# Kernel tuning notes

Measured on AMD Instinct MI355X. Metric: run time of the kernel, lower is better.

Reference implementation:

```python
import jax, jax.numpy as jnp
import numpy as np

N_HEAD = 16
HEAD_DIM = 128  # n_embd // n_head
EPS = 1e-6
ROPE_BASE = 10000.0


def rmsnorm(x, w):
    rms = jnp.mean(x * x, axis=-1, keepdims=True)
    return w * (x * jax.lax.rsqrt(rms + EPS))


def rope_cache(T, head_dim):
    half = head_dim // 2
    inv_freq = 1.0 / (ROPE_BASE ** (jnp.arange(half, dtype=jnp.float32) / half))
    pos = jnp.arange(T, dtype=jnp.float32)
    freqs = pos[:, None] * inv_freq[None, :]  # [T, half]
    return jnp.cos(freqs), jnp.sin(freqs)


def apply_rope(x, cos, sin):
    # x: [B, H, T, D]; cos/sin: [T, D/2]
    half = x.shape[-1] // 2
    x1, x2 = x[..., :half], x[..., half:]
    return jnp.concatenate([x1 * cos - x2 * sin, x1 * sin + x2 * cos], axis=-1)


def setup_inputs() -> dict:
    key = jax.random.key(0)
    ks = jax.random.split(key, 8)
    B, T, C, Hid = 2, 2048, 2048, 5632
    s = 0.02
    return {
        "x": jax.random.normal(ks[0], (B, T, C), dtype=jnp.float32),
        "w_norm1": jnp.ones((C,), dtype=jnp.float32),
        "w_qkv": jax.random.normal(ks[1], (C, 3 * C), dtype=jnp.float32) * s,
        "w_proj": jax.random.normal(ks[2], (C, C), dtype=jnp.float32) * s,
        "w_norm2": jnp.ones((C,), dtype=jnp.float32),
        "w1": jax.random.normal(ks[3], (C, Hid), dtype=jnp.float32) * s,
        "w2": jax.random.normal(ks[4], (C, Hid), dtype=jnp.float32) * s,
        "w3": jax.random.normal(ks[5], (Hid, C), dtype=jnp.float32) * s,
    }


def reference(x, w_norm1, w_qkv, w_proj, w_norm2, w1, w2, w3):
    B, T, C = x.shape
    H, D = N_HEAD, HEAD_DIM

    # ---- attention branch ----
    h = rmsnorm(x, w_norm1)
    qkv = h @ w_qkv  # [B, T, 3C]
    q, k, v = jnp.split(qkv, 3, axis=-1)
    q = q.reshape(B, T, H, D).transpose(0, 2, 1, 3)  # [B,H,T,D]
    k = k.reshape(B, T, H, D).transpose(0, 2, 1, 3)
    v = v.reshape(B, T, H, D).transpose(0, 2, 1, 3)

    cos, sin = rope_cache(T, D)
    q = apply_rope(q, cos, sin)
    k = apply_rope(k, cos, sin)

    att = jnp.einsum('bhqd,bhkd->bhqk', q, k) / np.sqrt(D).astype(np.float32)
    causal = jnp.tril(jnp.ones((T, T), dtype=bool))
    att = jnp.where(causal, att, -jnp.inf)
    att = jax.nn.softmax(att, axis=-1)
    out = jnp.einsum('bhqk,bhkd->bhqd', att, v)
    out = out.transpose(0, 2, 1, 3).reshape(B, T, C)
    x = x + out @ w_proj

    # ---- SwiGLU MLP branch ----
    h2 = rmsnorm(x, w_norm2)
    x = x + (jax.nn.silu(h2 @ w1) * (h2 @ w2)) @ w3
    return x
```

## Files before the change

kernel.cpp:

```cpp
#include <hip/hip_runtime.h>

typedef short s16x8 __attribute__((ext_vector_type(8)));
typedef unsigned short u16;
typedef u16 u16x8 __attribute__((ext_vector_type(8)));
typedef u16 u16x4 __attribute__((ext_vector_type(4)));
typedef float f32x4 __attribute__((ext_vector_type(4)));

#define DEVINL __device__ __forceinline__

DEVINL u16 f2bf(float f) {
    unsigned u = __float_as_uint(f);
    u += 0x7FFFu + ((u >> 16) & 1u);
    return (u16)(u >> 16);
}
DEVINL float bf2f(u16 h) { return __uint_as_float((unsigned)h << 16); }

DEVINL void gl2lds16(const void* g, void* l) {
    __builtin_amdgcn_global_load_lds((const __attribute__((address_space(1))) void*)g,
                                     (__attribute__((address_space(3))) void*)l, 16, 0, 0);
}

__global__ __launch_bounds__(256) void tcast(
    const float* __restrict__ src, u16* __restrict__ dst, const int K, const int N)
{
    __shared__ float tile[32][33];
    const long k0 = (long)blockIdx.x * 32;
    const long n0 = (long)blockIdx.y * 32;
    const int tid = threadIdx.x;
    const int r = tid >> 3, c4 = (tid & 7) * 4;
    float4 v = *(const float4*)&src[(k0 + r) * N + n0 + c4];
    tile[r][c4] = v.x; tile[r][c4 + 1] = v.y; tile[r][c4 + 2] = v.z; tile[r][c4 + 3] = v.w;
    __syncthreads();
    u16x4 ov;
    ov[0] = f2bf(tile[c4][r]);     ov[1] = f2bf(tile[c4 + 1][r]);
    ov[2] = f2bf(tile[c4 + 2][r]); ov[3] = f2bf(tile[c4 + 3][r]);
    *(u16x4*)&dst[(n0 + r) * K + k0 + c4] = ov;
}

__global__ __launch_bounds__(256) void rmsnorm_cast(
    const float* __restrict__ x, const float* __restrict__ wn, u16* __restrict__ out)
{
    const int C = 2048;
    const long row = blockIdx.x;
    const int tid = threadIdx.x;
    const float4* xr = (const float4*)(x + row * C);
    float4 a = xr[tid * 2], b = xr[tid * 2 + 1];
    float ss = a.x*a.x + a.y*a.y + a.z*a.z + a.w*a.w
             + b.x*b.x + b.y*b.y + b.z*b.z + b.w*b.w;
#pragma unroll
    for (int m = 1; m < 64; m <<= 1) ss += __shfl_xor(ss, m);
    __shared__ float red[4];
    if ((tid & 63) == 0) red[tid >> 6] = ss;
    __syncthreads();
    float scale = rsqrtf((red[0] + red[1] + red[2] + red[3]) * (1.f / 2048.f) + 1e-6f);
    const float4* wr = (const float4*)wn;
    float4 wa = wr[tid * 2], wb = wr[tid * 2 + 1];
    u16x8 o;
    o[0] = f2bf(a.x * scale * wa.x); o[1] = f2bf(a.y * scale * wa.y);
    o[2] = f2bf(a.z * scale * wa.z); o[3] = f2bf(a.w * scale * wa.w);
    o[4] = f2bf(b.x * scale * wb.x); o[5] = f2bf(b.y * scale * wb.y);
    o[6] = f2bf(b.z * scale * wb.z); o[7] = f2bf(b.w * scale * wb.w);
    *(u16x8*)&out[row * C + tid * 8] = o;
}

template <int MODE>
__global__ __launch_bounds__(256, 2) void gemm128(
    const u16* __restrict__ A, const u16* __restrict__ Bt,
    const int N, const int K,
    float* __restrict__ outF, u16* __restrict__ outB,
    const float* __restrict__ resid)
{
    __shared__ u16 As[128 * 64];
    __shared__ u16 Bs[128 * 64];
    const int tid = threadIdx.x;
    const int lane = tid & 63;
    const int w = tid >> 6;
    const int wm = w >> 1, wn = w & 1;
    const int quad = lane >> 4, l16 = lane & 15;
    const long m0 = (long)blockIdx.x * 128;
    const long n0 = (long)blockIdx.y * 128;

    const u16* ga[4]; const u16* gb[4]; char* la[4]; char* lb[4];
#pragma unroll
    for (int rr = 0; rr < 4; ++rr) {
        int idx = rr * 256 + tid;
        int r = idx >> 3, j = idx & 7;
        int c = (j ^ (r & 7)) * 8;
        ga[rr] = A + (m0 + r) * K + c;
        gb[rr] = Bt + (n0 + r) * K + c;
        la[rr] = (char*)As + idx * 16;
        lb[rr] = (char*)Bs + idx * 16;
    }

    f32x4 acc[4][4] = {};

    for (int k0 = 0; k0 < K; k0 += 64) {
#pragma unroll
        for (int rr = 0; rr < 4; ++rr) {
            gl2lds16(ga[rr] + k0, la[rr]);
            gl2lds16(gb[rr] + k0, lb[rr]);
        }
        __syncthreads();
#pragma unroll
        for (int ks = 0; ks < 2; ++ks) {
            s16x8 af[4], bfv[4];
#pragma unroll
            for (int mt = 0; mt < 4; ++mt)
                af[mt] = *(const s16x8*)&As[(wm * 64 + mt * 16 + l16) * 64 +
                                            ((ks * 4 + quad) ^ (l16 & 7)) * 8];
#pragma unroll
            for (int nt = 0; nt < 4; ++nt)
                bfv[nt] = *(const s16x8*)&Bs[(wn * 64 + nt * 16 + l16) * 64 +
                                             ((ks * 4 + quad) ^ (l16 & 7)) * 8];
#pragma unroll
            for (int mt = 0; mt < 4; ++mt)
#pragma unroll
                for (int nt = 0; nt < 4; ++nt)
                    acc[mt][nt] = __builtin_amdgcn_mfma_f32_16x16x32_bf16(af[mt], bfv[nt], acc[mt][nt], 0, 0, 0);
        }
        __syncthreads();
    }

#pragma unroll
    for (int mt = 0; mt < 4; ++mt)
#pragma unroll
        for (int reg = 0; reg < 4; ++reg) {
            long row = m0 + wm * 64 + mt * 16 + quad * 4 + reg;
#pragma unroll
            for (int nt = 0; nt < 4; ++nt) {
                long col = n0 + wn * 64 + nt * 16 + l16;
                float v = acc[mt][nt][reg];
                if (MODE == 0) {
                    outB[row * N + col] = f2bf(v);
                } else {
                    outF[row * N + col] = resid[row * N + col] + v;
                }
            }
        }
}

__global__ __launch_bounds__(256, 2) void gemm_ffn(
    const u16* __restrict__ A, const u16* __restrict__ B1t, const u16* __restrict__ B2t,
    const int N, const int K, u16* __restrict__ outB)
{
    __shared__ u16 As[128 * 64];
    __shared__ u16 B1s[128 * 64];
    __shared__ u16 B2s[128 * 64];
    const int tid = threadIdx.x;
    const int lane = tid & 63;
    const int w = tid >> 6;
    const int wm = w >> 1, wn = w & 1;
    const int quad = lane >> 4, l16 = lane & 15;
    const long m0 = (long)blockIdx.x * 128;
    const long n0 = (long)blockIdx.y * 128;

    const u16* ga[4]; const u16* gb1[4]; const u16* gb2[4];
    char* la[4]; char* lb1[4]; char* lb2[4];
#pragma unroll
    for (int rr = 0; rr < 4; ++rr) {
        int idx = rr * 256 + tid;
        int r = idx >> 3, j = idx & 7;
        int c = (j ^ (r & 7)) * 8;
        ga[rr]  = A + (m0 + r) * K + c;
        gb1[rr] = B1t + (n0 + r) * K + c;
        gb2[rr] = B2t + (n0 + r) * K + c;
        la[rr]  = (char*)As + idx * 16;
        lb1[rr] = (char*)B1s + idx * 16;
        lb2[rr] = (char*)B2s + idx * 16;
    }

    f32x4 acc1[4][4] = {};
    f32x4 acc2[4][4] = {};

    for (int k0 = 0; k0 < K; k0 += 64) {
#pragma unroll
        for (int rr = 0; rr < 4; ++rr) {
            gl2lds16(ga[rr] + k0, la[rr]);
            gl2lds16(gb1[rr] + k0, lb1[rr]);
            gl2lds16(gb2[rr] + k0, lb2[rr]);
        }
        __syncthreads();
#pragma unroll
        for (int ks = 0; ks < 2; ++ks) {
            s16x8 af[4], b1f[4], b2f[4];
#pragma unroll
            for (int mt = 0; mt < 4; ++mt)
                af[mt] = *(const s16x8*)&As[(wm * 64 + mt * 16 + l16) * 64 +
                                            ((ks * 4 + quad) ^ (l16 & 7)) * 8];
#pragma unroll
            for (int nt = 0; nt < 4; ++nt) {
                b1f[nt] = *(const s16x8*)&B1s[(wn * 64 + nt * 16 + l16) * 64 +
                                              ((ks * 4 + quad) ^ (l16 & 7)) * 8];
                b2f[nt] = *(const s16x8*)&B2s[(wn * 64 + nt * 16 + l16) * 64 +
                                              ((ks * 4 + quad) ^ (l16 & 7)) * 8];
            }
#pragma unroll
            for (int mt = 0; mt < 4; ++mt)
#pragma unroll
                for (int nt = 0; nt < 4; ++nt) {
                    acc1[mt][nt] = __builtin_amdgcn_mfma_f32_16x16x32_bf16(af[mt], b1f[nt], acc1[mt][nt], 0, 0, 0);
                    acc2[mt][nt] = __builtin_amdgcn_mfma_f32_16x16x32_bf16(af[mt], b2f[nt], acc2[mt][nt], 0, 0, 0);
                }
        }
        __syncthreads();
    }

#pragma unroll
    for (int mt = 0; mt < 4; ++mt)
#pragma unroll
        for (int reg = 0; reg < 4; ++reg) {
            long row = m0 + wm * 64 + mt * 16 + quad * 4 + reg;
#pragma unroll
            for (int nt = 0; nt < 4; ++nt) {
                long col = n0 + wn * 64 + nt * 16 + l16;
                float g = acc1[mt][nt][reg];
                float s = g / (1.f + __expf(-g));
                outB[row * N + col] = f2bf(s * acc2[mt][nt][reg]);
            }
        }
}

__global__ __launch_bounds__(256) void rope_qk(
    const u16* __restrict__ qkv, u16* __restrict__ qT, u16* __restrict__ kT)
{
    const int row = blockIdx.x;
    const int t = row & 2047, b = row >> 11;
    const int tid = threadIdx.x;
    __shared__ u16 buf[4096];
    const u16* src = qkv + (long)row * 6144;
    u16x8 aa = *(const u16x8*)&src[tid * 8];
    u16x8 kk = *(const u16x8*)&src[2048 + tid * 8];
    *(u16x8*)&buf[tid * 8] = aa;
    *(u16x8*)&buf[2048 + tid * 8] = kk;
    __syncthreads();
    const int c = tid * 8;
    const int h = c >> 7, dh = c & 127;
    const bool first = dh < 64;
    const int pc = first ? (c + 64) : (c - 64);
    float cs[8], sn[8];
#pragma unroll
    for (int j = 0; j < 8; ++j) {
        float inv = __expf(-(float)((dh & 63) + j) * 0.14391156831212787f);
        float ang = (float)t * inv;
        cs[j] = cosf(ang); sn[j] = sinf(ang);
    }
    const long obase = ((long)(b * 16 + h) * 2048 + t) * 128 + dh;
#pragma unroll
    for (int part = 0; part < 2; ++part) {
        const int base = part * 2048;
        u16x8 mine = *(const u16x8*)&buf[base + c];
        u16x8 oth  = *(const u16x8*)&buf[base + pc];
        const float qs = part ? 1.f : 0.08838834764831845f;
        u16x8 o;
#pragma unroll
        for (int j = 0; j < 8; ++j) {
            float xv = bf2f(mine[j]), yv = bf2f(oth[j]);
            float ov = first ? (xv * cs[j] - yv * sn[j]) : (yv * sn[j] + xv * cs[j]);
            o[j] = f2bf(ov * qs);
        }
        u16* dst = part ? kT : qT;
        *(u16x8*)&dst[obase] = o;
    }
}

__global__ __launch_bounds__(256) void vtrans(
    const u16* __restrict__ qkv, u16* __restrict__ vT)
{
    const int bh = blockIdx.x;
    const int b = bh >> 4, h = bh & 15;
    const int t0 = blockIdx.y * 64, d0 = blockIdx.z * 64;
    __shared__ u16 tile[64 * 65];
    const int tid = threadIdx.x;
#pragma unroll
    for (int rr = 0; rr < 2; ++rr) {
        int idx = rr * 256 + tid;
        int r = idx >> 3, c = (idx & 7) * 8;
        u16x8 v = *(const u16x8*)&qkv[(long)(b * 2048 + t0 + r) * 6144 + 4096 + h * 128 + d0 + c];
#pragma unroll
        for (int j = 0; j < 8; ++j) tile[r * 65 + c + j] = v[j];
    }
    __syncthreads();
#pragma unroll
    for (int rr = 0; rr < 2; ++rr) {
        int idx = rr * 256 + tid;
        int dd = idx >> 3, cc = (idx & 7) * 8;
        u16x8 o;
#pragma unroll
        for (int j = 0; j < 8; ++j) o[j] = tile[(cc + j) * 65 + dd];
        *(u16x8*)&vT[((long)bh * 128 + d0 + dd) * 2048 + t0 + cc] = o;
    }
}

__global__ __launch_bounds__(256, 2) void attn_kernel(
    const u16* __restrict__ qT, const u16* __restrict__ kT,
    const u16* __restrict__ vT, u16* __restrict__ outT)
{
    const int T = 2048, D = 128;
    const int qt = gridDim.x - 1 - blockIdx.x;
    const int bh = blockIdx.y;
    const int tid = threadIdx.x, lane = tid & 63, w = tid >> 6;
    const int quad = lane >> 4, l16 = lane & 15;
    const int qrow = qt * 64 + w * 16;

    __shared__ u16 Ks[2][64 * 128];
    __shared__ u16 Vs[2][128 * 64];
    __shared__ u16 Ps[4][16 * 64];

    s16x8 aq[4];
    const u16* qb = qT + ((long)bh * T + qrow + l16) * D;
#pragma unroll
    for (int kk = 0; kk < 4; ++kk)
        aq[kk] = *(const s16x8*)&qb[kk * 32 + quad * 8];

    f32x4 o[8] = {};
    float mi[4] = {-INFINITY, -INFINITY, -INFINITY, -INFINITY};
    float li[4] = {0.f, 0.f, 0.f, 0.f};

    const u16* kg0 = kT + (long)bh * T * D;
    const u16* vg0 = vT + (long)bh * D * T;

    auto stage = [&](int kt, int b) {
        const int k0 = kt * 64;
#pragma unroll
        for (int rr = 0; rr < 4; ++rr) {
            int idx = rr * 256 + tid;
            int kr = idx >> 4, kj = idx & 15;
            gl2lds16(kg0 + (long)(k0 + kr) * D + ((kj ^ (kr & 15)) * 8),
                     (char*)Ks[b] + idx * 16);
            int vr = idx >> 3, vj = idx & 7;
            gl2lds16(vg0 + (long)vr * T + k0 + ((vj ^ (vr & 7)) * 8),
                     (char*)Vs[b] + idx * 16);
        }
    };

    stage(0, 0);

    for (int kt = 0; kt <= qt; ++kt) {
        __syncthreads();
        if (kt < qt) stage(kt + 1, (kt + 1) & 1);
        const u16* ks_ = Ks[kt & 1];
        const u16* vs_ = Vs[kt & 1];
        const int k0 = kt * 64;

        f32x4 sf[4] = {};
#pragma unroll
        for (int kk = 0; kk < 4; ++kk) {
#pragma unroll
            for (int nt = 0; nt < 4; ++nt) {
                s16x8 kb = *(const s16x8*)&ks_[(nt * 16 + l16) * 128 +
                                               ((kk * 4 + quad) ^ (l16 & 15)) * 8];
                sf[nt] = __builtin_amdgcn_mfma_f32_16x16x32_bf16(aq[kk], kb, sf[nt], 0, 0, 0);
            }
        }

        float S[4][4];
        if (kt == qt) {
#pragma unroll
            for (int nt = 0; nt < 4; ++nt) {
                int col = k0 + nt * 16 + l16;
#pragma unroll
                for (int reg = 0; reg < 4; ++reg) {
                    int row = qrow + quad * 4 + reg;
                    S[nt][reg] = (col <= row) ? sf[nt][reg] : -INFINITY;
                }
            }
        } else {
#pragma unroll
            for (int nt = 0; nt < 4; ++nt)
#pragma unroll
                for (int reg = 0; reg < 4; ++reg)
                    S[nt][reg] = sf[nt][reg];
        }

        float rm[4];
#pragma unroll
        for (int reg = 0; reg < 4; ++reg)
            rm[reg] = fmaxf(fmaxf(S[0][reg], S[1][reg]), fmaxf(S[2][reg], S[3][reg]));
#pragma unroll
        for (int m = 1; m < 16; m <<= 1)
#pragma unroll
            for (int reg = 0; reg < 4; ++reg)
                rm[reg] = fmaxf(rm[reg], __shfl_xor(rm[reg], m));

        float alpha[4], rs[4];
#pragma unroll
        for (int reg = 0; reg < 4; ++reg) {
            float mn = fmaxf(mi[reg], rm[reg]);
            alpha[reg] = __expf(mi[reg] - mn);
            mi[reg] = mn;
            rs[reg] = 0.f;
        }
#pragma unroll
        for (int nt = 0; nt < 4; ++nt)
#pragma unroll
            for (int reg = 0; reg < 4; ++reg) {
                float p = __expf(S[nt][reg] - mi[reg]);
                S[nt][reg] = p;
                rs[reg] += p;
            }
#pragma unroll
        for (int m = 1; m < 16; m <<= 1)
#pragma unroll
            for (int reg = 0; reg < 4; ++reg)
                rs[reg] += __shfl_xor(rs[reg], m);
#pragma unroll
        for (int reg = 0; reg < 4; ++reg)
            li[reg] = li[reg] * alpha[reg] + rs[reg];
#pragma unroll
        for (int dt = 0; dt < 8; ++dt)
#pragma unroll
            for (int reg = 0; reg < 4; ++reg)
                o[dt][reg] *= alpha[reg];

#pragma unroll
        for (int nt = 0; nt < 4; ++nt)
#pragma unroll
            for (int reg = 0; reg < 4; ++reg) {
                int prow = quad * 4 + reg;
                int pcol = nt * 16 + l16;
                Ps[w][prow * 64 + (((pcol >> 3) ^ (prow & 7)) * 8) + (pcol & 7)]
                    = f2bf(S[nt][reg]);
            }

#pragma unroll
        for (int ks = 0; ks < 2; ++ks) {
            s16x8 pa = *(const s16x8*)&Ps[w][l16 * 64 +
                                             ((ks * 4 + quad) ^ (l16 & 7)) * 8];
#pragma unroll
            for (int dt = 0; dt < 8; ++dt) {
                s16x8 vb = *(const s16x8*)&vs_[(dt * 16 + l16) * 64 +
                                               ((ks * 4 + quad) ^ (l16 & 7)) * 8];
                o[dt] = __builtin_amdgcn_mfma_f32_16x16x32_bf16(pa, vb, o[dt], 0, 0, 0);
            }
        }
    }

    const int b = bh >> 4, h = bh & 15;
#pragma unroll
    for (int reg = 0; reg < 4; ++reg) {
        float inv = 1.f / li[reg];
        int t = qrow + quad * 4 + reg;
        u16* orow = outT + ((long)(b * T + t)) * 2048 + h * 128;
#pragma unroll
        for (int dt = 0; dt < 8; ++dt)
            orow[dt * 16 + l16] = f2bf(o[dt][reg] * inv);
    }
}

extern "C" void kernel_launch(void* const* d_in, const int* in_sizes, int n_in,
                              void* d_out, int out_size, void* d_ws, size_t ws_size,
                              hipStream_t stream) {
    const float* x      = (const float*)d_in[0];
    const float* wn1    = (const float*)d_in[1];
    const float* w_qkv  = (const float*)d_in[2];
    const float* w_proj = (const float*)d_in[3];
    const float* wn2    = (const float*)d_in[4];
    const float* w1     = (const float*)d_in[5];
    const float* w2     = (const float*)d_in[6];
    const float* w3     = (const float*)d_in[7];
    float* out = (float*)d_out;

    char* p = (char*)d_ws;
    u16* Z       = (u16*)p; p += (size_t)6144 * 2048 * 2;
    u16* wproj_t = (u16*)p; p += (size_t)2048 * 2048 * 2;
    u16* w1_t    = (u16*)p; p += (size_t)5632 * 2048 * 2;
    u16* w2_t    = (u16*)p; p += (size_t)5632 * 2048 * 2;
    u16* C       = (u16*)p; p += (size_t)4096 * 2048 * 2;
    u16* D       = (u16*)p; p += (size_t)4096 * 6144 * 2;
    u16* E       = (u16*)p; p += (size_t)3 * 32 * 2048 * 128 * 2;

    u16* wqkv_t = Z;
    u16* w3_t   = Z;
    u16* qT = E;
    u16* kT = E + (size_t)32 * 2048 * 128;
    u16* vT = E + (size_t)2 * 32 * 2048 * 128;
    float* x2 = (float*)E;
    u16* uu = D;

    tcast<<<dim3(64, 192), 256, 0, stream>>>(w_qkv, wqkv_t, 2048, 6144);
    tcast<<<dim3(64, 64), 256, 0, stream>>>(w_proj, wproj_t, 2048, 2048);
    tcast<<<dim3(64, 176), 256, 0, stream>>>(w1, w1_t, 2048, 5632);
    tcast<<<dim3(64, 176), 256, 0, stream>>>(w2, w2_t, 2048, 5632);

    rmsnorm_cast<<<4096, 256, 0, stream>>>(x, wn1, C);
    gemm128<0><<<dim3(32, 48), 256, 0, stream>>>(C, wqkv_t, 6144, 2048,
                                                 nullptr, D, nullptr);
    rope_qk<<<4096, 256, 0, stream>>>(D, qT, kT);
    vtrans<<<dim3(32, 32, 2), 256, 0, stream>>>(D, vT);

    tcast<<<dim3(176, 64), 256, 0, stream>>>(w3, w3_t, 5632, 2048);

    attn_kernel<<<dim3(32, 32), 256, 0, stream>>>(qT, kT, vT, C);

    gemm128<1><<<dim3(32, 16), 256, 0, stream>>>(C, wproj_t, 2048, 2048,
                                                 x2, nullptr, x);
    rmsnorm_cast<<<4096, 256, 0, stream>>>(x2, wn2, C);
    gemm_ffn<<<dim3(32, 44), 256, 0, stream>>>(C, w1_t, w2_t, 5632, 2048, uu);
    gemm128<1><<<dim3(32, 16), 256, 0, stream>>>(uu, w3_t, 2048, 5632,
                                                 out, nullptr, x2);
}
```

Before: 871.1 us.

## Enlarge GEMM tiles to 256x128 with 512 threads and multi-buffered LDS prefetch

Replaces the 128x128, 256-thread GEMM kernels with 256x128 tiles run by 8 waves. The LDS is now triple-buffered (plain GEMM) or double-buffered (FFN GEMM), and global-to-LDS loads for the next k-tiles are issued before the MFMA blocks. The MFMA work is split into two halves separated by explicit barriers, waitcnt and setprio so that LDS reads, global prefetch and matrix math overlap. This targets the load-then-sync stalls of the old single-buffer loop, at the cost of more LDS per block, which may limit occupancy, and fewer blocks per launch.

```diff
diff --git a/kernel.cpp b/kernel.cpp
--- a/kernel.cpp
+++ b/kernel.cpp
@@ -19,6 +19,14 @@
     __builtin_amdgcn_global_load_lds((const __attribute__((address_space(1))) void*)g,
                                      (__attribute__((address_space(3))) void*)l, 16, 0, 0);
 }
+
+DEVINL f32x4 mfma16(s16x8 a, s16x8 b, f32x4 c) {
+    return __builtin_amdgcn_mfma_f32_16x16x32_bf16(a, b, c, 0, 0, 0);
+}
+
+#define SBAR()   __builtin_amdgcn_s_barrier()
+#define SCHEDB() __builtin_amdgcn_sched_barrier(0)
+#define WLGKM0() do { asm volatile("s_waitcnt lgkmcnt(0)"); __builtin_amdgcn_sched_barrier(0); } while (0)
 
 __global__ __launch_bounds__(256) void tcast(
     const float* __restrict__ src, u16* __restrict__ dst, const int K, const int N)
@@ -64,61 +72,118 @@
 }
 
 template <int MODE>
-__global__ __launch_bounds__(256, 2) void gemm128(
+__global__ __launch_bounds__(512, 2) void gemm256(
     const u16* __restrict__ A, const u16* __restrict__ Bt,
     const int N, const int K,
     float* __restrict__ outF, u16* __restrict__ outB,
     const float* __restrict__ resid)
 {
-    __shared__ u16 As[128 * 64];
-    __shared__ u16 Bs[128 * 64];
+    __shared__ u16 As[3][256 * 64];
+    __shared__ u16 Bs[3][128 * 64];
     const int tid = threadIdx.x;
     const int lane = tid & 63;
     const int w = tid >> 6;
     const int wm = w >> 1, wn = w & 1;
     const int quad = lane >> 4, l16 = lane & 15;
-    const long m0 = (long)blockIdx.x * 128;
+    const long m0 = (long)blockIdx.x * 256;
     const long n0 = (long)blockIdx.y * 128;
 
-    const u16* ga[4]; const u16* gb[4]; char* la[4]; char* lb[4];
-#pragma unroll
-    for (int rr = 0; rr < 4; ++rr) {
-        int idx = rr * 256 + tid;
-        int r = idx >> 3, j = idx & 7;
-        int c = (j ^ (r & 7)) * 8;
-        ga[rr] = A + (m0 + r) * K + c;
-        gb[rr] = Bt + (n0 + r) * K + c;
-        la[rr] = (char*)As + idx * 16;
-        lb[rr] = (char*)Bs + idx * 16;
-    }
+    const u16* ga[4]; const u16* gb[2];
+    int lofA[4], lofB[2];
+#pragma unroll
+    for (int r = 0; r < 4; ++r) {
+        int idx = r * 512 + tid;
+        int row = idx >> 3, j = idx & 7;
+        int c = (j ^ (row & 7)) * 8;
+        ga[r] = A + (m0 + row) * K + c;
+        lofA[r] = idx * 16;
+    }
+#pragma unroll
+    for (int r = 0; r < 2; ++r) {
+        int idx = r * 512 + tid;
+        int row = idx >> 3, j = idx & 7;
+        int c = (j ^ (row & 7)) * 8;
+        gb[r] = Bt + (n0 + row) * K + c;
+        lofB[r] = idx * 16;
+    }
+
+    auto stage = [&](int buf, int k0) {
+#pragma unroll
+        for (int r = 0; r < 4; ++r)
+            gl2lds16(ga[r] + k0, (char*)As[buf] + lofA[r]);
+#pragma unroll
+        for (int r = 0; r < 2; ++r)
+            gl2lds16(gb[r] + k0, (char*)Bs[buf] + lofB[r]);
+    };
 
     f32x4 acc[4][4] = {};
 
-    for (int k0 = 0; k0 < K; k0 += 64) {
-#pragma unroll
-        for (int rr = 0; rr < 4; ++rr) {
-            gl2lds16(ga[rr] + k0, la[rr]);
-            gl2lds16(gb[rr] + k0, lb[rr]);
-        }
-        __syncthreads();
-#pragma unroll
-        for (int ks = 0; ks < 2; ++ks) {
-            s16x8 af[4], bfv[4];
-#pragma unroll
-            for (int mt = 0; mt < 4; ++mt)
-                af[mt] = *(const s16x8*)&As[(wm * 64 + mt * 16 + l16) * 64 +
-                                            ((ks * 4 + quad) ^ (l16 & 7)) * 8];
-#pragma unroll
-            for (int nt = 0; nt < 4; ++nt)
-                bfv[nt] = *(const s16x8*)&Bs[(wn * 64 + nt * 16 + l16) * 64 +
-                                             ((ks * 4 + quad) ^ (l16 & 7)) * 8];
-#pragma unroll
-            for (int mt = 0; mt < 4; ++mt)
-#pragma unroll
-                for (int nt = 0; nt < 4; ++nt)
-                    acc[mt][nt] = __builtin_amdgcn_mfma_f32_16x16x32_bf16(af[mt], bfv[nt], acc[mt][nt], 0, 0, 0);
-        }
-        __syncthreads();
+    const int NT = K >> 6;
+    stage(0, 0);
+    stage(1, 64);
+    asm volatile("s_waitcnt vmcnt(6)" ::: "memory");
+    SBAR();
+
+    int cur = 0;
+    for (int t = 0; t < NT; ++t) {
+        const u16* as_ = As[cur];
+        const u16* bs_ = Bs[cur];
+        const bool pf = (t + 2 < NT);
+        int nb = cur + 2; if (nb >= 3) nb -= 3;
+
+        s16x8 af[4][2], bf[2][2];
+#pragma unroll
+        for (int mt = 0; mt < 4; ++mt)
+#pragma unroll
+            for (int ks = 0; ks < 2; ++ks)
+                af[mt][ks] = *(const s16x8*)&as_[(wm * 64 + mt * 16 + l16) * 64 +
+                                                 ((ks * 4 + quad) ^ (l16 & 7)) * 8];
+#pragma unroll
+        for (int nt = 0; nt < 2; ++nt)
+#pragma unroll
+            for (int ks = 0; ks < 2; ++ks)
+                bf[nt][ks] = *(const s16x8*)&bs_[(wn * 64 + nt * 16 + l16) * 64 +
+                                                 ((ks * 4 + quad) ^ (l16 & 7)) * 8];
+        if (pf) stage(nb, (t + 2) << 6);
+        SCHEDB();
+        SBAR();
+        WLGKM0();
+        __builtin_amdgcn_s_setprio(1);
+#pragma unroll
+        for (int mt = 0; mt < 4; ++mt)
+#pragma unroll
+            for (int nt = 0; nt < 2; ++nt)
+#pragma unroll
+                for (int ks = 0; ks < 2; ++ks)
+                    acc[mt][nt] = mfma16(af[mt][ks], bf[nt][ks], acc[mt][nt]);
+        __builtin_amdgcn_s_setprio(0);
+        SCHEDB();
+        SBAR();
+
+        s16x8 bg[2][2];
+#pragma unroll
+        for (int nt = 0; nt < 2; ++nt)
+#pragma unroll
+            for (int ks = 0; ks < 2; ++ks)
+                bg[nt][ks] = *(const s16x8*)&bs_[(wn * 64 + (nt + 2) * 16 + l16) * 64 +
+                                                 ((ks * 4 + quad) ^ (l16 & 7)) * 8];
+        SCHEDB();
+        SBAR();
+        WLGKM0();
+        __builtin_amdgcn_s_setprio(1);
+#pragma unroll
+        for (int mt = 0; mt < 4; ++mt)
+#pragma unroll
+            for (int nt = 0; nt < 2; ++nt)
+#pragma unroll
+                for (int ks = 0; ks < 2; ++ks)
+                    acc[mt][nt + 2] = mfma16(af[mt][ks], bg[nt][ks], acc[mt][nt + 2]);
+        __builtin_amdgcn_s_setprio(0);
+        if (pf) asm volatile("s_waitcnt vmcnt(6)" ::: "memory");
+        else    asm volatile("s_waitcnt vmcnt(0)" ::: "memory");
+        SCHEDB();
+        SBAR();
+        cur = (cur == 2) ? 0 : cur + 1;
     }
 
 #pragma unroll
@@ -139,70 +204,127 @@
         }
 }
 
-__global__ __launch_bounds__(256, 2) void gemm_ffn(
+__global__ __launch_bounds__(512, 2) void gemm_ffn256(
     const u16* __restrict__ A, const u16* __restrict__ B1t, const u16* __restrict__ B2t,
     const int N, const int K, u16* __restrict__ outB)
 {
-    __shared__ u16 As[128 * 64];
-    __shared__ u16 B1s[128 * 64];
-    __shared__ u16 B2s[128 * 64];
+    __shared__ u16 As[2][256 * 64];
+    __shared__ u16 B1s[2][128 * 64];
+    __shared__ u16 B2s[2][128 * 64];
     const int tid = threadIdx.x;
     const int lane = tid & 63;
     const int w = tid >> 6;
     const int wm = w >> 1, wn = w & 1;
     const int quad = lane >> 4, l16 = lane & 15;
-    const long m0 = (long)blockIdx.x * 128;
+    const long m0 = (long)blockIdx.x * 256;
     const long n0 = (long)blockIdx.y * 128;
 
-    const u16* ga[4]; const u16* gb1[4]; const u16* gb2[4];
-    char* la[4]; char* lb1[4]; char* lb2[4];
-#pragma unroll
-    for (int rr = 0; rr < 4; ++rr) {
-        int idx = rr * 256 + tid;
-        int r = idx >> 3, j = idx & 7;
-        int c = (j ^ (r & 7)) * 8;
-        ga[rr]  = A + (m0 + r) * K + c;
-        gb1[rr] = B1t + (n0 + r) * K + c;
-        gb2[rr] = B2t + (n0 + r) * K + c;
-        la[rr]  = (char*)As + idx * 16;
-        lb1[rr] = (char*)B1s + idx * 16;
-        lb2[rr] = (char*)B2s + idx * 16;
-    }
+    const u16* ga[4]; const u16* gb1[2]; const u16* gb2[2];
+    int lofA[4], lofB[2];
+#pragma unroll
+    for (int r = 0; r < 4; ++r) {
+        int idx = r * 512 + tid;
+        int row = idx >> 3, j = idx & 7;
+        int c = (j ^ (row & 7)) * 8;
+        ga[r] = A + (m0 + row) * K + c;
+        lofA[r] = idx * 16;
+    }
+#pragma unroll
+    for (int r = 0; r < 2; ++r) {
+        int idx = r * 512 + tid;
+        int row = idx >> 3, j = idx & 7;
+        int c = (j ^ (row & 7)) * 8;
+        gb1[r] = B1t + (n0 + row) * K + c;
+        gb2[r] = B2t + (n0 + row) * K + c;
+        lofB[r] = idx * 16;
+    }
+
+    auto stage = [&](int buf, int k0) {
+#pragma unroll
+        for (int r = 0; r < 4; ++r)
+            gl2lds16(ga[r] + k0, (char*)As[buf] + lofA[r]);
+#pragma unroll
+        for (int r = 0; r < 2; ++r) {
+            gl2lds16(gb1[r] + k0, (char*)B1s[buf] + lofB[r]);
+            gl2lds16(gb2[r] + k0, (char*)B2s[buf] + lofB[r]);
+        }
+    };
 
     f32x4 acc1[4][4] = {};
     f32x4 acc2[4][4] = {};
 
-    for (int k0 = 0; k0 < K; k0 += 64) {
-#pragma unroll
-        for (int rr = 0; rr < 4; ++rr) {
-            gl2lds16(ga[rr] + k0, la[rr]);
-            gl2lds16(gb1[rr] + k0, lb1[rr]);
-            gl2lds16(gb2[rr] + k0, lb2[rr]);
-        }
-        __syncthreads();
-#pragma unroll
-        for (int ks = 0; ks < 2; ++ks) {
-            s16x8 af[4], b1f[4], b2f[4];
-#pragma unroll
-            for (int mt = 0; mt < 4; ++mt)
-                af[mt] = *(const s16x8*)&As[(wm * 64 + mt * 16 + l16) * 64 +
-                                            ((ks * 4 + quad) ^ (l16 & 7)) * 8];
-#pragma unroll
-            for (int nt = 0; nt < 4; ++nt) {
-                b1f[nt] = *(const s16x8*)&B1s[(wn * 64 + nt * 16 + l16) * 64 +
-                                              ((ks * 4 + quad) ^ (l16 & 7)) * 8];
-                b2f[nt] = *(const s16x8*)&B2s[(wn * 64 + nt * 16 + l16) * 64 +
-                                              ((ks * 4 + quad) ^ (l16 & 7)) * 8];
-            }
-#pragma unroll
-            for (int mt = 0; mt < 4; ++mt)
-#pragma unroll
-                for (int nt = 0; nt < 4; ++nt) {
-                    acc1[mt][nt] = __builtin_amdgcn_mfma_f32_16x16x32_bf16(af[mt], b1f[nt], acc1[mt][nt], 0, 0, 0);
-                    acc2[mt][nt] = __builtin_amdgcn_mfma_f32_16x16x32_bf16(af[mt], b2f[nt], acc2[mt][nt], 0, 0, 0);
+    const int NT = K >> 6;
+    stage(0, 0);
+    asm volatile("s_waitcnt vmcnt(0)" ::: "memory");
+    SBAR();
+
+    for (int t = 0; t < NT; ++t) {
+        const int cur = t & 1;
+        const u16* as_ = As[cur];
+        const u16* b1_ = B1s[cur];
+        const u16* b2_ = B2s[cur];
+
+        s16x8 af[4][2], b1f[2][2], b2f[2][2];
+#pragma unroll
+        for (int mt = 0; mt < 4; ++mt)
+#pragma unroll
+            for (int ks = 0; ks < 2; ++ks)
+                af[mt][ks] = *(const s16x8*)&as_[(wm * 64 + mt * 16 + l16) * 64 +
+                                                 ((ks * 4 + quad) ^ (l16 & 7)) * 8];
+#pragma unroll
+        for (int nt = 0; nt < 2; ++nt)
+#pragma unroll
+            for (int ks = 0; ks < 2; ++ks) {
+                b1f[nt][ks] = *(const s16x8*)&b1_[(wn * 64 + nt * 16 + l16) * 64 +
+                                                  ((ks * 4 + quad) ^ (l16 & 7)) * 8];
+                b2f[nt][ks] = *(const s16x8*)&b2_[(wn * 64 + nt * 16 + l16) * 64 +
+                                                  ((ks * 4 + quad) ^ (l16 & 7)) * 8];
+            }
+        if (t + 1 < NT) stage(cur ^ 1, (t + 1) << 6);
+        SCHEDB();
+        SBAR();
+        WLGKM0();
+        __builtin_amdgcn_s_setprio(1);
+#pragma unroll
+        for (int mt = 0; mt < 4; ++mt)
+#pragma unroll
+            for (int nt = 0; nt < 2; ++nt)
+#pragma unroll
+                for (int ks = 0; ks < 2; ++ks) {
+                    acc1[mt][nt] = mfma16(af[mt][ks], b1f[nt][ks], acc1[mt][nt]);
+                    acc2[mt][nt] = mfma16(af[mt][ks], b2f[nt][ks], acc2[mt][nt]);
                 }
-        }
-        __syncthreads();
+        __builtin_amdgcn_s_setprio(0);
+        SCHEDB();
+        SBAR();
+
+        s16x8 b1g[2][2], b2g[2][2];
+#pragma unroll
+        for (int nt = 0; nt < 2; ++nt)
+#pragma unroll
+            for (int ks = 0; ks < 2; ++ks) {
+                b1g[nt][ks] = *(const s16x8*)&b1_[(wn * 64 + (nt + 2) * 16 + l16) * 64 +
+                                                  ((ks * 4 + quad) ^ (l16 & 7)) * 8];
+                b2g[nt][ks] = *(const s16x8*)&b2_[(wn * 64 + (nt + 2) * 16 + l16) * 64 +
+                                                  ((ks * 4 + quad) ^ (l16 & 7)) * 8];
+            }
+        SCHEDB();
+        SBAR();
+        WLGKM0();
+        __builtin_amdgcn_s_setprio(1);
+#pragma unroll
+        for (int mt = 0; mt < 4; ++mt)
+#pragma unroll
+            for (int nt = 0; nt < 2; ++nt)
+#pragma unroll
+                for (int ks = 0; ks < 2; ++ks) {
+                    acc1[mt][nt + 2] = mfma16(af[mt][ks], b1g[nt][ks], acc1[mt][nt + 2]);
+                    acc2[mt][nt + 2] = mfma16(af[mt][ks], b2g[nt][ks], acc2[mt][nt + 2]);
+                }
+        __builtin_amdgcn_s_setprio(0);
+        asm volatile("s_waitcnt vmcnt(0)" ::: "memory");
+        SCHEDB();
+        SBAR();
     }
 
 #pragma unroll
@@ -483,7 +605,7 @@
     tcast<<<dim3(64, 176), 256, 0, stream>>>(w2, w2_t, 2048, 5632);
 
     rmsnorm_cast<<<4096, 256, 0, stream>>>(x, wn1, C);
-    gemm128<0><<<dim3(32, 48), 256, 0, stream>>>(C, wqkv_t, 6144, 2048,
+    gemm256<0><<<dim3(16, 48), 512, 0, stream>>>(C, wqkv_t, 6144, 2048,
                                                  nullptr, D, nullptr);
     rope_qk<<<4096, 256, 0, stream>>>(D, qT, kT);
     vtrans<<<dim3(32, 32, 2), 256, 0, stream>>>(D, vT);
@@ -492,10 +614,10 @@
 
     attn_kernel<<<dim3(32, 32), 256, 0, stream>>>(qT, kT, vT, C);
 
-    gemm128<1><<<dim3(32, 16), 256, 0, stream>>>(C, wproj_t, 2048, 2048,
+    gemm256<1><<<dim3(16, 16), 512, 0, stream>>>(C, wproj_t, 2048, 2048,
                                                  x2, nullptr, x);
     rmsnorm_cast<<<4096, 256, 0, stream>>>(x2, wn2, C);
-    gemm_ffn<<<dim3(32, 44), 256, 0, stream>>>(C, w1_t, w2_t, 5632, 2048, uu);
-    gemm128<1><<<dim3(32, 16), 256, 0, stream>>>(uu, w3_t, 2048, 5632,
+    gemm_ffn256<<<dim3(16, 44), 512, 0, stream>>>(C, w1_t, w2_t, 5632, 2048, uu);
+    gemm256<1><<<dim3(16, 16), 512, 0, stream>>>(uu, w3_t, 2048, 5632,
                                                  out, nullptr, x2);
 }
```

Result: slower. 943.4 us (+8.3%).

## Replace GEMMs with 8-wave 256x128 double-buffered pipelined kernels

Applied to the files above, without the earlier changes.

Rewrites the bf16 GEMM and fused SwiGLU GEMM as 512-thread kernels computing 256x128 tiles. Operand tiles are double-buffered in LDS, and direct global-to-LDS prefetches are interleaved with MFMA phases using explicit barriers, waitcnt, sched barriers and setprio. This aims to hide global load latency and raise MFMA utilization compared with the single-buffered load/sync/compute loop. In exchange, grids are smaller, LDS and register use per block are higher, and the hand-tuned wait counts are fragile.

```diff
diff --git a/kernel.cpp b/kernel.cpp
--- a/kernel.cpp
+++ b/kernel.cpp
@@ -19,6 +19,15 @@
     __builtin_amdgcn_global_load_lds((const __attribute__((address_space(1))) void*)g,
                                      (__attribute__((address_space(3))) void*)l, 16, 0, 0);
 }
+
+DEVINL f32x4 mfma16(s16x8 a, s16x8 b, f32x4 c) {
+    return __builtin_amdgcn_mfma_f32_16x16x32_bf16(a, b, c, 0, 0, 0);
+}
+
+#define SBAR()   __builtin_amdgcn_s_barrier()
+#define SCHEDB() __builtin_amdgcn_sched_barrier(0)
+#define WLGKM0() do { asm volatile("s_waitcnt lgkmcnt(0)"); __builtin_amdgcn_sched_barrier(0); } while (0)
+#define WVM(n)   do { asm volatile("s_waitcnt vmcnt(" #n ")" ::: "memory"); __builtin_amdgcn_sched_barrier(0); } while (0)
 
 __global__ __launch_bounds__(256) void tcast(
     const float* __restrict__ src, u16* __restrict__ dst, const int K, const int N)
@@ -64,71 +73,137 @@
 }
 
 template <int MODE>
-__global__ __launch_bounds__(256, 2) void gemm128(
+__global__ __launch_bounds__(512, 2) void gemm8p(
     const u16* __restrict__ A, const u16* __restrict__ Bt,
     const int N, const int K,
     float* __restrict__ outF, u16* __restrict__ outB,
     const float* __restrict__ resid)
 {
-    __shared__ u16 As[128 * 64];
-    __shared__ u16 Bs[128 * 64];
+    __shared__ u16 As[2][2][128 * 64];
+    __shared__ u16 Bs[2][128 * 64];
     const int tid = threadIdx.x;
     const int lane = tid & 63;
     const int w = tid >> 6;
-    const int wm = w >> 1, wn = w & 1;
+    const int wm = w >> 2, wn = w & 3;
     const int quad = lane >> 4, l16 = lane & 15;
-    const long m0 = (long)blockIdx.x * 128;
+    const long m0 = (long)blockIdx.x * 256;
     const long n0 = (long)blockIdx.y * 128;
 
-    const u16* ga[4]; const u16* gb[4]; char* la[4]; char* lb[4];
-#pragma unroll
-    for (int rr = 0; rr < 4; ++rr) {
-        int idx = rr * 256 + tid;
-        int r = idx >> 3, j = idx & 7;
-        int c = (j ^ (r & 7)) * 8;
-        ga[rr] = A + (m0 + r) * K + c;
-        gb[rr] = Bt + (n0 + r) * K + c;
-        la[rr] = (char*)As + idx * 16;
-        lb[rr] = (char*)Bs + idx * 16;
-    }
-
-    f32x4 acc[4][4] = {};
-
-    for (int k0 = 0; k0 < K; k0 += 64) {
-#pragma unroll
-        for (int rr = 0; rr < 4; ++rr) {
-            gl2lds16(ga[rr] + k0, la[rr]);
-            gl2lds16(gb[rr] + k0, lb[rr]);
-        }
-        __syncthreads();
-#pragma unroll
-        for (int ks = 0; ks < 2; ++ks) {
-            s16x8 af[4], bfv[4];
-#pragma unroll
-            for (int mt = 0; mt < 4; ++mt)
-                af[mt] = *(const s16x8*)&As[(wm * 64 + mt * 16 + l16) * 64 +
-                                            ((ks * 4 + quad) ^ (l16 & 7)) * 8];
-#pragma unroll
-            for (int nt = 0; nt < 4; ++nt)
-                bfv[nt] = *(const s16x8*)&Bs[(wn * 64 + nt * 16 + l16) * 64 +
-                                             ((ks * 4 + quad) ^ (l16 & 7)) * 8];
-#pragma unroll
-            for (int mt = 0; mt < 4; ++mt)
-#pragma unroll
-                for (int nt = 0; nt < 4; ++nt)
-                    acc[mt][nt] = __builtin_amdgcn_mfma_f32_16x16x32_bf16(af[mt], bfv[nt], acc[mt][nt], 0, 0, 0);
-        }
-        __syncthreads();
-    }
-
-#pragma unroll
-    for (int mt = 0; mt < 4; ++mt)
+    const int idx0 = tid, idx1 = 512 + tid;
+    const int r0 = idx0 >> 3, r1 = idx1 >> 3;
+    const u16* gA0 = A + (m0 + r0) * K + ((idx0 & 7) ^ (r0 & 7)) * 8;
+    const u16* gA1 = A + (m0 + r1) * K + ((idx1 & 7) ^ (r1 & 7)) * 8;
+    const u16* gB0 = Bt + (n0 + r0) * K + ((idx0 & 7) ^ (r0 & 7)) * 8;
+    const u16* gB1 = Bt + (n0 + r1) * K + ((idx1 & 7) ^ (r1 & 7)) * 8;
+    const long hstep = (long)128 * K;
+
+    auto stageA = [&](int buf, int h, int k) {
+        gl2lds16(gA0 + h * hstep + k, (char*)&As[buf][h][0] + idx0 * 16);
+        gl2lds16(gA1 + h * hstep + k, (char*)&As[buf][h][0] + idx1 * 16);
+    };
+    auto stageB = [&](int buf, int k) {
+        gl2lds16(gB0 + k, (char*)&Bs[buf][0] + idx0 * 16);
+        gl2lds16(gB1 + k, (char*)&Bs[buf][0] + idx1 * 16);
+    };
+
+    const int arow = l16;
+    const int asw  = l16 & 7;
+    const int brow = wn * 32 + l16;
+
+    f32x4 acc[8][2] = {};
+    const int NT = K >> 6, NI = NT >> 1;
+
+    stageA(0, 0, 0); stageA(0, 1, 0); stageB(0, 0);
+    stageA(1, 0, 64); stageA(1, 1, 64); stageB(1, 64);
+    WVM(6);
+    SBAR();
+
+    for (int j = 0; j < NI; ++j) {
+        const int k0 = j << 7;
+        const bool pf = (j + 1 < NI);
+
+#pragma unroll
+        for (int half = 0; half < 2; ++half) {
+            const u16* as_ = &As[half][wm][0];
+            const u16* bs_ = &Bs[half][0];
+            s16x8 a0[4][2], a1[4][2], b0[2], b1[2];
+
+#pragma unroll
+            for (int mt = 0; mt < 4; ++mt)
+#pragma unroll
+                for (int ks = 0; ks < 2; ++ks)
+                    a0[mt][ks] = *(const s16x8*)&as_[(mt * 16 + arow) * 64 +
+                                                     ((ks * 4 + quad) ^ asw) * 8];
+#pragma unroll
+            for (int nt = 0; nt < 2; ++nt)
+                b0[nt] = *(const s16x8*)&bs_[(brow + nt * 16) * 64 + (quad ^ asw) * 8];
+            if (half == 0) { if (j >= 1) stageB(1, k0 + 64); }
+            else           { if (pf)     stageB(0, k0 + 128); }
+            SCHEDB(); SBAR(); WLGKM0();
+            __builtin_amdgcn_s_setprio(1);
+#pragma unroll
+            for (int mt = 0; mt < 4; ++mt)
+#pragma unroll
+                for (int nt = 0; nt < 2; ++nt)
+                    acc[mt][nt] = mfma16(a0[mt][0], b0[nt], acc[mt][nt]);
+            __builtin_amdgcn_s_setprio(0);
+            SCHEDB(); SBAR();
+
+#pragma unroll
+            for (int mt = 0; mt < 4; ++mt)
+#pragma unroll
+                for (int ks = 0; ks < 2; ++ks)
+                    a1[mt][ks] = *(const s16x8*)&as_[((mt + 4) * 16 + arow) * 64 +
+                                                     ((ks * 4 + quad) ^ asw) * 8];
+            SCHEDB(); SBAR(); WLGKM0();
+            __builtin_amdgcn_s_setprio(1);
+#pragma unroll
+            for (int mt = 0; mt < 4; ++mt)
+#pragma unroll
+                for (int nt = 0; nt < 2; ++nt)
+                    acc[mt + 4][nt] = mfma16(a1[mt][0], b0[nt], acc[mt + 4][nt]);
+            __builtin_amdgcn_s_setprio(0);
+            SCHEDB(); SBAR();
+
+#pragma unroll
+            for (int nt = 0; nt < 2; ++nt)
+                b1[nt] = *(const s16x8*)&bs_[(brow + nt * 16) * 64 + ((4 + quad) ^ asw) * 8];
+            if (half == 0) { if (pf) stageA(0, 0, k0 + 128); }
+            else           { if (pf) stageA(1, 0, k0 + 192); }
+            SCHEDB(); SBAR(); WLGKM0();
+            __builtin_amdgcn_s_setprio(1);
+#pragma unroll
+            for (int mt = 0; mt < 4; ++mt)
+#pragma unroll
+                for (int nt = 0; nt < 2; ++nt)
+                    acc[mt][nt] = mfma16(a0[mt][1], b1[nt], acc[mt][nt]);
+            __builtin_amdgcn_s_setprio(0);
+            SCHEDB(); SBAR();
+
+            if (half == 0) { if (pf) stageA(0, 1, k0 + 128); }
+            else           { if (pf) stageA(1, 1, k0 + 192); }
+            SCHEDB(); SBAR();
+            __builtin_amdgcn_s_setprio(1);
+#pragma unroll
+            for (int mt = 0; mt < 4; ++mt)
+#pragma unroll
+                for (int nt = 0; nt < 2; ++nt)
+                    acc[mt + 4][nt] = mfma16(a1[mt][1], b1[nt], acc[mt + 4][nt]);
+            __builtin_amdgcn_s_setprio(0);
+            if (half == 0) { if (pf) { WVM(4); } else { WVM(0); } }
+            else           { WVM(4); }
+            SCHEDB(); SBAR();
+        }
+    }
+
+#pragma unroll
+    for (int mt = 0; mt < 8; ++mt)
 #pragma unroll
         for (int reg = 0; reg < 4; ++reg) {
-            long row = m0 + wm * 64 + mt * 16 + quad * 4 + reg;
-#pragma unroll
-            for (int nt = 0; nt < 4; ++nt) {
-                long col = n0 + wn * 64 + nt * 16 + l16;
+            long row = m0 + wm * 128 + mt * 16 + quad * 4 + reg;
+#pragma unroll
+            for (int nt = 0; nt < 2; ++nt) {
+                long col = n0 + wn * 32 + nt * 16 + l16;
                 float v = acc[mt][nt][reg];
                 if (MODE == 0) {
                     outB[row * N + col] = f2bf(v);
@@ -139,80 +214,159 @@
         }
 }
 
-__global__ __launch_bounds__(256, 2) void gemm_ffn(
+__global__ __launch_bounds__(512, 2) void gemm8p_ffn(
     const u16* __restrict__ A, const u16* __restrict__ B1t, const u16* __restrict__ B2t,
     const int N, const int K, u16* __restrict__ outB)
 {
-    __shared__ u16 As[128 * 64];
-    __shared__ u16 B1s[128 * 64];
-    __shared__ u16 B2s[128 * 64];
+    __shared__ u16 As[2][2][128 * 64];
+    __shared__ u16 B1s[2][128 * 64];
+    __shared__ u16 B2s[2][128 * 64];
     const int tid = threadIdx.x;
     const int lane = tid & 63;
     const int w = tid >> 6;
-    const int wm = w >> 1, wn = w & 1;
+    const int wm = w >> 2, wn = w & 3;
     const int quad = lane >> 4, l16 = lane & 15;
-    const long m0 = (long)blockIdx.x * 128;
+    const long m0 = (long)blockIdx.x * 256;
     const long n0 = (long)blockIdx.y * 128;
 
-    const u16* ga[4]; const u16* gb1[4]; const u16* gb2[4];
-    char* la[4]; char* lb1[4]; char* lb2[4];
-#pragma unroll
-    for (int rr = 0; rr < 4; ++rr) {
-        int idx = rr * 256 + tid;
-        int r = idx >> 3, j = idx & 7;
-        int c = (j ^ (r & 7)) * 8;
-        ga[rr]  = A + (m0 + r) * K + c;
-        gb1[rr] = B1t + (n0 + r) * K + c;
-        gb2[rr] = B2t + (n0 + r) * K + c;
-        la[rr]  = (char*)As + idx * 16;
-        lb1[rr] = (char*)B1s + idx * 16;
-        lb2[rr] = (char*)B2s + idx * 16;
-    }
-
-    f32x4 acc1[4][4] = {};
-    f32x4 acc2[4][4] = {};
-
-    for (int k0 = 0; k0 < K; k0 += 64) {
-#pragma unroll
-        for (int rr = 0; rr < 4; ++rr) {
-            gl2lds16(ga[rr] + k0, la[rr]);
-            gl2lds16(gb1[rr] + k0, lb1[rr]);
-            gl2lds16(gb2[rr] + k0, lb2[rr]);
-        }
-        __syncthreads();
-#pragma unroll
-        for (int ks = 0; ks < 2; ++ks) {
-            s16x8 af[4], b1f[4], b2f[4];
-#pragma unroll
-            for (int mt = 0; mt < 4; ++mt)
-                af[mt] = *(const s16x8*)&As[(wm * 64 + mt * 16 + l16) * 64 +
-                                            ((ks * 4 + quad) ^ (l16 & 7)) * 8];
-#pragma unroll
-            for (int nt = 0; nt < 4; ++nt) {
-                b1f[nt] = *(const s16x8*)&B1s[(wn * 64 + nt * 16 + l16) * 64 +
-                                              ((ks * 4 + quad) ^ (l16 & 7)) * 8];
-                b2f[nt] = *(const s16x8*)&B2s[(wn * 64 + nt * 16 + l16) * 64 +
-                                              ((ks * 4 + quad) ^ (l16 & 7)) * 8];
-            }
-#pragma unroll
-            for (int mt = 0; mt < 4; ++mt)
-#pragma unroll
-                for (int nt = 0; nt < 4; ++nt) {
-                    acc1[mt][nt] = __builtin_amdgcn_mfma_f32_16x16x32_bf16(af[mt], b1f[nt], acc1[mt][nt], 0, 0, 0);
-                    acc2[mt][nt] = __builtin_amdgcn_mfma_f32_16x16x32_bf16(af[mt], b2f[nt], acc2[mt][nt], 0, 0, 0);
+    const int idx0 = tid, idx1 = 512 + tid;
+    const int r0 = idx0 >> 3, r1 = idx1 >> 3;
+    const int sw0 = ((idx0 & 7) ^ (r0 & 7)) * 8, sw1 = ((idx1 & 7) ^ (r1 & 7)) * 8;
+    const u16* gA0 = A + (m0 + r0) * K + sw0;
+    const u16* gA1 = A + (m0 + r1) * K + sw1;
+    const u16* gB10 = B1t + (n0 + r0) * K + sw0;
+    const u16* gB11 = B1t + (n0 + r1) * K + sw1;
+    const u16* gB20 = B2t + (n0 + r0) * K + sw0;
+    const u16* gB21 = B2t + (n0 + r1) * K + sw1;
+    const long hstep = (long)128 * K;
+
+    auto stageA = [&](int buf, int h, int k) {
+        gl2lds16(gA0 + h * hstep + k, (char*)&As[buf][h][0] + idx0 * 16);
+        gl2lds16(gA1 + h * hstep + k, (char*)&As[buf][h][0] + idx1 * 16);
+    };
+    auto stageB1 = [&](int buf, int k) {
+        gl2lds16(gB10 + k, (char*)&B1s[buf][0] + idx0 * 16);
+        gl2lds16(gB11 + k, (char*)&B1s[buf][0] + idx1 * 16);
+    };
+    auto stageB2 = [&](int buf, int k) {
+        gl2lds16(gB20 + k, (char*)&B2s[buf][0] + idx0 * 16);
+        gl2lds16(gB21 + k, (char*)&B2s[buf][0] + idx1 * 16);
+    };
+
+    const int arow = l16;
+    const int asw  = l16 & 7;
+    const int brow = wn * 32 + l16;
+
+    f32x4 acc1[8][2] = {};
+    f32x4 acc2[8][2] = {};
+    const int NT = K >> 6, NI = NT >> 1;
+
+    stageA(0, 0, 0); stageA(0, 1, 0); stageB1(0, 0); stageB2(0, 0);
+    stageA(1, 0, 64); stageA(1, 1, 64); stageB1(1, 64); stageB2(1, 64);
+    WVM(8);
+    SBAR();
+
+    for (int j = 0; j < NI; ++j) {
+        const int k0 = j << 7;
+        const bool pf = (j + 1 < NI);
+
+#pragma unroll
+        for (int half = 0; half < 2; ++half) {
+            const u16* as_ = &As[half][wm][0];
+            const u16* c1_ = &B1s[half][0];
+            const u16* c2_ = &B2s[half][0];
+            s16x8 a0[4][2], a1[4][2], b10[2], b20[2], b11[2], b21[2];
+
+#pragma unroll
+            for (int mt = 0; mt < 4; ++mt)
+#pragma unroll
+                for (int ks = 0; ks < 2; ++ks)
+                    a0[mt][ks] = *(const s16x8*)&as_[(mt * 16 + arow) * 64 +
+                                                     ((ks * 4 + quad) ^ asw) * 8];
+#pragma unroll
+            for (int nt = 0; nt < 2; ++nt) {
+                b10[nt] = *(const s16x8*)&c1_[(brow + nt * 16) * 64 + (quad ^ asw) * 8];
+                b20[nt] = *(const s16x8*)&c2_[(brow + nt * 16) * 64 + (quad ^ asw) * 8];
+            }
+            if (half == 0) { if (j >= 1) stageB1(1, k0 + 64); }
+            else           { if (pf)     stageB1(0, k0 + 128); }
+            SCHEDB(); SBAR(); WLGKM0();
+            __builtin_amdgcn_s_setprio(1);
+#pragma unroll
+            for (int mt = 0; mt < 4; ++mt)
+#pragma unroll
+                for (int nt = 0; nt < 2; ++nt) {
+                    acc1[mt][nt] = mfma16(a0[mt][0], b10[nt], acc1[mt][nt]);
+                    acc2[mt][nt] = mfma16(a0[mt][0], b20[nt], acc2[mt][nt]);
                 }
-        }
-        __syncthreads();
-    }
-
-#pragma unroll
-    for (int mt = 0; mt < 4; ++mt)
+            __builtin_amdgcn_s_setprio(0);
+            SCHEDB(); SBAR();
+
+#pragma unroll
+            for (int mt = 0; mt < 4; ++mt)
+#pragma unroll
+                for (int ks = 0; ks < 2; ++ks)
+                    a1[mt][ks] = *(const s16x8*)&as_[((mt + 4) * 16 + arow) * 64 +
+                                                     ((ks * 4 + quad) ^ asw) * 8];
+            if (half == 0) { if (j >= 1) stageB2(1, k0 + 64); }
+            else           { if (pf)     stageB2(0, k0 + 128); }
+            SCHEDB(); SBAR(); WLGKM0();
+            __builtin_amdgcn_s_setprio(1);
+#pragma unroll
+            for (int mt = 0; mt < 4; ++mt)
+#pragma unroll
+                for (int nt = 0; nt < 2; ++nt) {
+                    acc1[mt + 4][nt] = mfma16(a1[mt][0], b10[nt], acc1[mt + 4][nt]);
+                    acc2[mt + 4][nt] = mfma16(a1[mt][0], b20[nt], acc2[mt + 4][nt]);
+                }
+            __builtin_amdgcn_s_setprio(0);
+            SCHEDB(); SBAR();
+
+#pragma unroll
+            for (int nt = 0; nt < 2; ++nt) {
+                b11[nt] = *(const s16x8*)&c1_[(brow + nt * 16) * 64 + ((4 + quad) ^ asw) * 8];
+                b21[nt] = *(const s16x8*)&c2_[(brow + nt * 16) * 64 + ((4 + quad) ^ asw) * 8];
+            }
+            if (half == 0) { if (pf) stageA(0, 0, k0 + 128); }
+            else           { if (pf) stageA(1, 0, k0 + 192); }
+            SCHEDB(); SBAR(); WLGKM0();
+            __builtin_amdgcn_s_setprio(1);
+#pragma unroll
+            for (int mt = 0; mt < 4; ++mt)
+#pragma unroll
+                for (int nt = 0; nt < 2; ++nt) {
+                    acc1[mt][nt] = mfma16(a0[mt][1], b11[nt], acc1[mt][nt]);
+                    acc2[mt][nt] = mfma16(a0[mt][1], b21[nt], acc2[mt][nt]);
+                }
+            __builtin_amdgcn_s_setprio(0);
+            SCHEDB(); SBAR();
+
+            if (half == 0) { if (pf) stageA(0, 1, k0 + 128); }
+            else           { if (pf) stageA(1, 1, k0 + 192); }
+            SCHEDB(); SBAR();
+            __builtin_amdgcn_s_setprio(1);
+#pragma unroll
+            for (int mt = 0; mt < 4; ++mt)
+#pragma unroll
+                for (int nt = 0; nt < 2; ++nt) {
+                    acc1[mt + 4][nt] = mfma16(a1[mt][1], b11[nt], acc1[mt + 4][nt]);
+                    acc2[mt + 4][nt] = mfma16(a1[mt][1], b21[nt], acc2[mt + 4][nt]);
+                }
+            __builtin_amdgcn_s_setprio(0);
+            if (half == 0) { if (pf) { WVM(4); } else { WVM(0); } }
+            else           { WVM(4); }
+            SCHEDB(); SBAR();
+        }
+    }
+
+#pragma unroll
+    for (int mt = 0; mt < 8; ++mt)
 #pragma unroll
         for (int reg = 0; reg < 4; ++reg) {
-            long row = m0 + wm * 64 + mt * 16 + quad * 4 + reg;
-#pragma unroll
-            for (int nt = 0; nt < 4; ++nt) {
-                long col = n0 + wn * 64 + nt * 16 + l16;
+            long row = m0 + wm * 128 + mt * 16 + quad * 4 + reg;
+#pragma unroll
+            for (int nt = 0; nt < 2; ++nt) {
+                long col = n0 + wn * 32 + nt * 16 + l16;
                 float g = acc1[mt][nt][reg];
                 float s = g / (1.f + __expf(-g));
                 outB[row * N + col] = f2bf(s * acc2[mt][nt][reg]);
@@ -483,8 +637,8 @@
     tcast<<<dim3(64, 176), 256, 0, stream>>>(w2, w2_t, 2048, 5632);
 
     rmsnorm_cast<<<4096, 256, 0, stream>>>(x, wn1, C);
-    gemm128<0><<<dim3(32, 48), 256, 0, stream>>>(C, wqkv_t, 6144, 2048,
-                                                 nullptr, D, nullptr);
+    gemm8p<0><<<dim3(16, 48), 512, 0, stream>>>(C, wqkv_t, 6144, 2048,
+                                                nullptr, D, nullptr);
     rope_qk<<<4096, 256, 0, stream>>>(D, qT, kT);
     vtrans<<<dim3(32, 32, 2), 256, 0, stream>>>(D, vT);
 
@@ -492,10 +646,10 @@
 
     attn_kernel<<<dim3(32, 32), 256, 0, stream>>>(qT, kT, vT, C);
 
-    gemm128<1><<<dim3(32, 16), 256, 0, stream>>>(C, wproj_t, 2048, 2048,
-                                                 x2, nullptr, x);
+    gemm8p<1><<<dim3(16, 16), 512, 0, stream>>>(C, wproj_t, 2048, 2048,
+                                                x2, nullptr, x);
     rmsnorm_cast<<<4096, 256, 0, stream>>>(x2, wn2, C);
-    gemm_ffn<<<dim3(32, 44), 256, 0, stream>>>(C, w1_t, w2_t, 5632, 2048, uu);
-    gemm128<1><<<dim3(32, 16), 256, 0, stream>>>(uu, w3_t, 2048, 5632,
-                                                 out, nullptr, x2);
-}
+    gemm8p_ffn<<<dim3(16, 44), 512, 0, stream>>>(C, w1_t, w2_t, 5632, 2048, uu);
+    gemm8p<1><<<dim3(16, 16), 512, 0, stream>>>(uu, w3_t, 2048, 5632,
+                                                out, nullptr, x2);
+}
```

New measurement: 1.179 ms. 35.4% more time.
